# Kernel optimization log

Hardware: AMD Instinct MI355X
Metric: run time of the kernel (lower is better)

The kernel has to match this reference:

```python
import jax, jax.numpy as jnp
import numpy as np

S, B, H, NH = 2048, 1, 2048, 16
HD = H // NH
ROTARY_BASE = 10000.0
MASK_FILL = -10000.0  # gpt2_attention_mask_func fill value


def _rotate_half(x):
    x1, x2 = jnp.split(x, 2, axis=-1)
    return jnp.concatenate((-x2, x1), axis=-1)


def _rotary_cos_sin(seq_len, dim, dtype):
    inv_freq = 1.0 / (ROTARY_BASE ** (jnp.arange(0, dim, 2, dtype=jnp.float32) / dim))
    t = jnp.arange(seq_len, dtype=jnp.float32)
    freqs = t[:, None] * inv_freq[None, :]          # [s, dim/2]
    emb = jnp.concatenate((freqs, freqs), axis=-1)  # [s, dim]
    # shape [s, 1, 1, dim] to broadcast over (batch, heads)
    return jnp.cos(emb)[:, None, None, :].astype(dtype), jnp.sin(emb)[:, None, None, :].astype(dtype)


def setup_inputs() -> dict:
    key = jax.random.key(0)
    k0, k1, k2 = jax.random.split(key, 3)
    hidden_states = jax.random.normal(k0, (S, B, H), dtype=jnp.float32) * 0.02
    # causal mask: True = masked (upper triangle above diagonal)
    attention_mask = jnp.triu(jnp.ones((1, 1, S, S), dtype=bool), k=1)
    w_qkv = jax.random.normal(k1, (3 * H, H), dtype=jnp.float32) * 0.02
    b_qkv = jnp.zeros((3 * H,), dtype=jnp.float32)
    w_dense = jax.random.normal(k2, (H, H), dtype=jnp.float32) * 0.02
    return {"hidden_states": hidden_states, "attention_mask": attention_mask,
            "w_qkv": w_qkv, "b_qkv": b_qkv, "w_dense": w_dense}


def reference(hidden_states, attention_mask, w_qkv, b_qkv, w_dense):
    s, b, h = hidden_states.shape
    # fused QKV projection: [s, b, 3h]
    mixed = jnp.einsum('sbh,oh->sbo', hidden_states, w_qkv) + b_qkv
    mixed = mixed.reshape(s, b, NH, 3 * HD)
    q, k, v = jnp.split(mixed, 3, axis=-1)  # each [s, b, nh, hd]
    # rotary embedding (rotary_pct == 1 -> full head dim)
    cos, sin = _rotary_cos_sin(s, HD, q.dtype)
    q = q * cos + _rotate_half(q) * sin
    k = k * cos + _rotate_half(k) * sin
    # scaled QK^T: [b, nh, sq, sk]
    norm_factor = jnp.asarray(1.0 / np.sqrt(HD), dtype=q.dtype)
    scores = jnp.einsum('sbnd,tbnd->bnst', q, k) * norm_factor
    scores = jnp.where(attention_mask, jnp.asarray(MASK_FILL, scores.dtype), scores)
    probs = jax.nn.softmax(scores.astype(jnp.float32), axis=-1).astype(scores.dtype)
    # PV: [s, b, nh, hd]
    ctx = jnp.einsum('bnst,tbnd->sbnd', probs, v)
    ctx = ctx.reshape(s, b, h)
    # RowParallelLinear with skip_bias_add: bias returned separately (not added)
    out = jnp.einsum('sbh,oh->sbo', ctx, w_dense)
    return out
```

## Files before the change

kernel.cpp:

```cpp
#include <hip/hip_runtime.h>


#define S_LEN 2048
#define NHEAD 16
#define HDIM  128
#define HID   2048
#define H3    6144

typedef short bf16x8 __attribute__((ext_vector_type(8)));
typedef float f32x4  __attribute__((ext_vector_type(4)));

__device__ __forceinline__ float bf2f(ushort u) {
  union { float f; unsigned int i; } v; v.i = ((unsigned int)u) << 16; return v.f;
}
__device__ __forceinline__ ushort f2bf(float f) {
  union { float f; unsigned int i; } v; v.f = f;
  unsigned int r = v.i + 0x7fffu + ((v.i >> 16) & 1u);
  return (ushort)(r >> 16);
}
__device__ __forceinline__ int4 cvt8(const float* p) {
  float4 a = *(const float4*)p, b = *(const float4*)(p + 4);
  union { ushort u[8]; int4 v; } r;
  r.u[0] = f2bf(a.x); r.u[1] = f2bf(a.y); r.u[2] = f2bf(a.z); r.u[3] = f2bf(a.w);
  r.u[4] = f2bf(b.x); r.u[5] = f2bf(b.y); r.u[6] = f2bf(b.z); r.u[7] = f2bf(b.w);
  return r.v;
}

typedef __attribute__((address_space(1))) const unsigned int gu32;
typedef __attribute__((address_space(3))) unsigned int lu32;
__device__ __forceinline__ void async16(const void* g, void* l) {
  __builtin_amdgcn_global_load_lds((gu32*)g, (lu32*)l, 16, 0, 0);
}

__global__ __launch_bounds__(256) void cvt_bf16(const float* __restrict__ src,
                                                ushort* __restrict__ dst, int n8) {
  int i = blockIdx.x * 256 + threadIdx.x;
  if (i < n8) *(int4*)&dst[(size_t)i * 8] = cvt8(&src[(size_t)i * 8]);
}

template<int BM, int BN, bool HAS_BIAS, bool OUT_F32>
__global__ __launch_bounds__(256) void gemm_async(const ushort* __restrict__ A,
                                                  const ushort* __restrict__ W,
                                                  const float* __restrict__ bias,
                                                  void* __restrict__ Cv,
                                                  int N, int K, int AS, int AH) {
  __shared__ __align__(16) ushort As[BM * 32];
  __shared__ __align__(16) ushort Ws[BN * 32];
  const int tid  = threadIdx.x;
  const int lane = tid & 63;
  const int w    = tid >> 6;
  const int wr   = w >> 1, wc = w & 1;
  const int quad = lane >> 4, ln15 = lane & 15;
  const int tm = blockIdx.y * BM, tn = blockIdx.x * BN;
  constexpr int MI = BM / 32, NJ = BN / 32;

  f32x4 acc[MI][NJ];
#pragma unroll
  for (int i = 0; i < MI; ++i)
#pragma unroll
    for (int j = 0; j < NJ; ++j) acc[i][j] = (f32x4){0.f, 0.f, 0.f, 0.f};

  const int lrow = lane >> 2;
  const int lcol = (lane & 3) * 8;

  for (int k0 = 0; k0 < K; k0 += 32) {
    const int aoff = (k0 >> 7) * AH + (k0 & 127) + lcol;
    for (int r = w; r < (BM + BN) / 16; r += 4) {
      if (r < BM / 16) {
        async16(&A[(size_t)(tm + r * 16 + lrow) * AS + aoff], &As[r * 16 * 32]);
      } else {
        const int rb = r - BM / 16;
        async16(&W[(size_t)(tn + rb * 16 + lrow) * K + k0 + lcol], &Ws[rb * 16 * 32]);
      }
    }
    __syncthreads();
    bf16x8 af[MI], bw[NJ];
#pragma unroll
    for (int i = 0; i < MI; ++i)
      af[i] = *(const bf16x8*)&As[((BM / 2) * wr + 16 * i + ln15) * 32 + quad * 8];
#pragma unroll
    for (int j = 0; j < NJ; ++j)
      bw[j] = *(const bf16x8*)&Ws[((BN / 2) * wc + 16 * j + ln15) * 32 + quad * 8];
#pragma unroll
    for (int i = 0; i < MI; ++i)
#pragma unroll
      for (int j = 0; j < NJ; ++j)
        acc[i][j] = __builtin_amdgcn_mfma_f32_16x16x32_bf16(af[i], bw[j], acc[i][j], 0, 0, 0);
    __syncthreads();
  }

#pragma unroll
  for (int i = 0; i < MI; ++i)
#pragma unroll
    for (int j = 0; j < NJ; ++j) {
      int col = tn + (BN / 2) * wc + 16 * j + ln15;
      float badd = HAS_BIAS ? bias[col] : 0.0f;
#pragma unroll
      for (int r = 0; r < 4; ++r) {
        int row = tm + (BM / 2) * wr + 16 * i + 4 * quad + r;
        float val = acc[i][j][r] + badd;
        if (OUT_F32) ((float*)Cv)[(size_t)row * N + col] = val;
        else         ((ushort*)Cv)[(size_t)row * N + col] = f2bf(val);
      }
    }
}

template<bool A_F32, bool HAS_BIAS, bool OUT_F32>
__global__ __launch_bounds__(256) void gemm_bt(const void* __restrict__ Av,
                                               const float* __restrict__ W,
                                               const float* __restrict__ bias,
                                               void* __restrict__ Cv,
                                               int M, int N, int K, int AS, int AH) {
  __shared__ __align__(16) ushort As[128 * 40];
  __shared__ __align__(16) ushort Ws[128 * 40];
  const int tid  = threadIdx.x;
  const int lane = tid & 63;
  const int w    = tid >> 6;
  const int wr   = w >> 1, wc = w & 1;
  const int quad = lane >> 4, ln15 = lane & 15;
  const int tm = blockIdx.y * 128, tn = blockIdx.x * 128;

  f32x4 acc[4][4];
#pragma unroll
  for (int i = 0; i < 4; ++i)
#pragma unroll
    for (int j = 0; j < 4; ++j) acc[i][j] = (f32x4){0.f, 0.f, 0.f, 0.f};

  const int row0 = tid >> 2, row1 = row0 + 64;
  const int kp   = (tid & 3) * 8;

  for (int k0 = 0; k0 < K; k0 += 32) {
    const int ka   = k0 + kp;
    const int aoff = (ka >> 7) * AH + (ka & 127);
    if (A_F32) {
      const float* A = (const float*)Av;
      *(int4*)&As[row0 * 40 + kp] = cvt8(&A[(size_t)(tm + row0) * AS + aoff]);
      *(int4*)&As[row1 * 40 + kp] = cvt8(&A[(size_t)(tm + row1) * AS + aoff]);
    } else {
      const ushort* A = (const ushort*)Av;
      *(int4*)&As[row0 * 40 + kp] = *(const int4*)&A[(size_t)(tm + row0) * AS + aoff];
      *(int4*)&As[row1 * 40 + kp] = *(const int4*)&A[(size_t)(tm + row1) * AS + aoff];
    }
    *(int4*)&Ws[row0 * 40 + kp] = cvt8(&W[(size_t)(tn + row0) * K + ka]);
    *(int4*)&Ws[row1 * 40 + kp] = cvt8(&W[(size_t)(tn + row1) * K + ka]);
    __syncthreads();
    bf16x8 af[4], bw[4];
#pragma unroll
    for (int i = 0; i < 4; ++i)
      af[i] = *(const bf16x8*)&As[(64 * wr + 16 * i + ln15) * 40 + quad * 8];
#pragma unroll
    for (int j = 0; j < 4; ++j)
      bw[j] = *(const bf16x8*)&Ws[(64 * wc + 16 * j + ln15) * 40 + quad * 8];
#pragma unroll
    for (int i = 0; i < 4; ++i)
#pragma unroll
      for (int j = 0; j < 4; ++j)
        acc[i][j] = __builtin_amdgcn_mfma_f32_16x16x32_bf16(af[i], bw[j], acc[i][j], 0, 0, 0);
    __syncthreads();
  }

#pragma unroll
  for (int i = 0; i < 4; ++i)
#pragma unroll
    for (int j = 0; j < 4; ++j) {
      int col = tn + 64 * wc + 16 * j + ln15;
      float badd = HAS_BIAS ? bias[col] : 0.0f;
#pragma unroll
      for (int r = 0; r < 4; ++r) {
        int row = tm + 64 * wr + 16 * i + 4 * quad + r;
        float val = acc[i][j][r] + badd;
        if (OUT_F32) ((float*)Cv)[(size_t)row * N + col] = val;
        else         ((ushort*)Cv)[(size_t)row * N + col] = f2bf(val);
      }
    }
}

__global__ __launch_bounds__(256) void rope_kernel(ushort* __restrict__ mixed) {
  int t = blockIdx.x * 256 + threadIdx.x;
  int d = t & 63;
  int n = (t >> 6) & (NHEAD - 1);
  int s = t >> 10;
  ushort* base = mixed + (size_t)s * H3 + n * 384;
  float invf = exp2f((float)d * (-13.287712379549449f / 64.0f));
  float ang = (float)s * invf;
  float si, c; sincosf(ang, &si, &c);
  float q0 = bf2f(base[d]),       q1 = bf2f(base[64 + d]);
  float k0 = bf2f(base[128 + d]), k1 = bf2f(base[192 + d]);
  base[d]       = f2bf(q0 * c - q1 * si);
  base[64 + d]  = f2bf(q1 * c + q0 * si);
  base[128 + d] = f2bf(k0 * c - k1 * si);
  base[192 + d] = f2bf(k1 * c + k0 * si);
}

__global__ __launch_bounds__(256) void v_transpose(const ushort* __restrict__ mixed,
                                                   ushort* __restrict__ vt) {
  __shared__ __align__(16) ushort Vl[64 * 136];
  const int tid = threadIdx.x;
  const int sb = blockIdx.x;
  const int n  = blockIdx.y;
#pragma unroll
  for (int it = 0; it < 4; ++it) {
    int c = tid + it * 256;
    int row = c >> 4, dp = (c & 15) * 8;
    *(int4*)&Vl[row * 136 + dp] =
        *(const int4*)&mixed[(size_t)(sb * 64 + row) * H3 + n * 384 + 256 + dp];
  }
  __syncthreads();
#pragma unroll
  for (int it = 0; it < 4; ++it) {
    int c = tid + it * 256;
    int d = c >> 3, sp = (c & 7) * 8;
    union { ushort u[8]; int4 v; } pk;
#pragma unroll
    for (int e = 0; e < 8; ++e) pk.u[e] = Vl[(sp + e) * 136 + d];
    *(int4*)&vt[((size_t)(n * 128 + d)) * S_LEN + sb * 64 + sp] = pk.v;
  }
}

__global__ __launch_bounds__(256) void attn_kernel(const ushort* __restrict__ mixed,
                                                   const ushort* __restrict__ vt,
                                                   ushort* __restrict__ ctx,
                                                   int CS, int CH) {
  __shared__ __align__(16) ushort Ks[64 * 136];
  __shared__ __align__(16) ushort Vt[128 * 72];
  __shared__ __align__(16) float  Ss[4 * 16 * 68];

  const int tid  = threadIdx.x;
  const int lane = tid & 63;
  const int w    = tid >> 6;
  const int quad = lane >> 4, ln15 = lane & 15;
  const int qb = blockIdx.x;
  const int n  = blockIdx.y;
  const float scale = 0.08838834764831845f;

  bf16x8 aqr[4];
#pragma unroll
  for (int ks = 0; ks < 4; ++ks)
    aqr[ks] = *(const bf16x8*)&mixed[(size_t)(qb * 64 + 16 * w + ln15) * H3 + n * 384
                                     + ks * 32 + quad * 8];

  f32x4 acc_o[8];
#pragma unroll
  for (int jt = 0; jt < 8; ++jt) acc_o[jt] = (f32x4){0.f, 0.f, 0.f, 0.f};
  float m_run[4], l_run[4];
#pragma unroll
  for (int r = 0; r < 4; ++r) { m_run[r] = -1e30f; l_run[r] = 0.0f; }

  float* Ssw = &Ss[w * 16 * 68];

  for (int kt = 0; kt <= qb; ++kt) {
#pragma unroll
    for (int it = 0; it < 4; ++it) {
      int c = tid + it * 256;
      int row = c >> 4, dp = (c & 15) * 8;
      *(int4*)&Ks[row * 136 + dp] =
          *(const int4*)&mixed[(size_t)(kt * 64 + row) * H3 + n * 384 + 128 + dp];
      int d = c >> 3, sp = (c & 7) * 8;
      *(int4*)&Vt[d * 72 + sp] =
          *(const int4*)&vt[((size_t)(n * 128 + d)) * S_LEN + kt * 64 + sp];
    }
    __syncthreads();

    f32x4 sacc[4];
#pragma unroll
    for (int jt = 0; jt < 4; ++jt) sacc[jt] = (f32x4){0.f, 0.f, 0.f, 0.f};
#pragma unroll
    for (int ks = 0; ks < 4; ++ks) {
#pragma unroll
      for (int jt = 0; jt < 4; ++jt) {
        bf16x8 bk = *(const bf16x8*)&Ks[(16 * jt + ln15) * 136 + ks * 32 + quad * 8];
        sacc[jt] = __builtin_amdgcn_mfma_f32_16x16x32_bf16(aqr[ks], bk, sacc[jt], 0, 0, 0);
      }
    }

    float sv[4][4];
    const int ig = qb * 64 + 16 * w + 4 * quad;
#pragma unroll
    for (int jt = 0; jt < 4; ++jt) {
      int jg = kt * 64 + 16 * jt + ln15;
#pragma unroll
      for (int r = 0; r < 4; ++r) {
        float x = sacc[jt][r] * scale;
        sv[jt][r] = (jg > ig + r) ? -10000.0f : x;
      }
    }

    float tmx[4];
#pragma unroll
    for (int r = 0; r < 4; ++r)
      tmx[r] = fmaxf(fmaxf(sv[0][r], sv[1][r]), fmaxf(sv[2][r], sv[3][r]));
#pragma unroll
    for (int m = 1; m <= 8; m <<= 1)
#pragma unroll
      for (int r = 0; r < 4; ++r) tmx[r] = fmaxf(tmx[r], __shfl_xor(tmx[r], m));

    float alpha[4];
#pragma unroll
    for (int r = 0; r < 4; ++r) {
      float m_new = fmaxf(m_run[r], tmx[r]);
      alpha[r] = __expf(m_run[r] - m_new);
      m_run[r] = m_new;
    }

    float ps[4] = {0.f, 0.f, 0.f, 0.f};
#pragma unroll
    for (int jt = 0; jt < 4; ++jt)
#pragma unroll
      for (int r = 0; r < 4; ++r) {
        float p = __expf(sv[jt][r] - m_run[r]);
        Ssw[(4 * quad + r) * 68 + 16 * jt + ln15] = p;
        ps[r] += p;
      }
#pragma unroll
    for (int m = 1; m <= 8; m <<= 1)
#pragma unroll
      for (int r = 0; r < 4; ++r) ps[r] += __shfl_xor(ps[r], m);
#pragma unroll
    for (int r = 0; r < 4; ++r) l_run[r] = alpha[r] * l_run[r] + ps[r];

#pragma unroll
    for (int jt = 0; jt < 8; ++jt)
#pragma unroll
      for (int r = 0; r < 4; ++r) acc_o[jt][r] *= alpha[r];
#pragma unroll
    for (int ks = 0; ks < 2; ++ks) {
      const float* pp = &Ssw[ln15 * 68 + ks * 32 + quad * 8];
      float4 p0 = *(const float4*)(pp);
      float4 p1 = *(const float4*)(pp + 4);
      bf16x8 ap;
      ap[0] = (short)f2bf(p0.x); ap[1] = (short)f2bf(p0.y);
      ap[2] = (short)f2bf(p0.z); ap[3] = (short)f2bf(p0.w);
      ap[4] = (short)f2bf(p1.x); ap[5] = (short)f2bf(p1.y);
      ap[6] = (short)f2bf(p1.z); ap[7] = (short)f2bf(p1.w);
#pragma unroll
      for (int jt = 0; jt < 8; ++jt) {
        bf16x8 bv = *(const bf16x8*)&Vt[(16 * jt + ln15) * 72 + ks * 32 + quad * 8];
        acc_o[jt] = __builtin_amdgcn_mfma_f32_16x16x32_bf16(ap, bv, acc_o[jt], 0, 0, 0);
      }
    }
    __syncthreads();
  }

  float rinv[4];
#pragma unroll
  for (int r = 0; r < 4; ++r) rinv[r] = 1.0f / l_run[r];
#pragma unroll
  for (int jt = 0; jt < 8; ++jt)
#pragma unroll
    for (int r = 0; r < 4; ++r) {
      int row = qb * 64 + 16 * w + 4 * quad + r;
      int col = 16 * jt + ln15;
      ctx[(size_t)row * CS + n * CH + col] = f2bf(acc_o[jt][r] * rinv[r]);
    }
}

extern "C" void kernel_launch(void* const* d_in, const int* in_sizes, int n_in,
                              void* d_out, int out_size, void* d_ws, size_t ws_size,
                              hipStream_t stream) {
  const float* hidden  = (const float*)d_in[0];
  const float* w_qkv   = (const float*)d_in[2];
  const float* b_qkv   = (const float*)d_in[3];
  const float* w_dense = (const float*)d_in[4];
  float* out = (float*)d_out;

  char* ws = (char*)d_ws;

  const size_t wq_b    = (size_t)H3 * HID * 2;
  const size_t h_b     = (size_t)S_LEN * HID * 2;
  const size_t mixed_b = (size_t)S_LEN * H3 * 2;
  const size_t vt_b    = (size_t)NHEAD * HDIM * S_LEN * 2;
  const size_t fast_need = wq_b + h_b + mixed_b + vt_b;

  if (ws_size >= fast_need) {
    ushort* WQ    = (ushort*)ws;
    ushort* Hbf   = (ushort*)(ws + wq_b);
    ushort* mixed = (ushort*)(ws + wq_b + h_b);
    ushort* vt    = (ushort*)(ws + wq_b + h_b + mixed_b);
    ushort* WD    = WQ;
    ushort* ctx   = mixed;

    cvt_bf16<<<2048, 256, 0, stream>>>(hidden, Hbf, S_LEN * HID / 8);
    cvt_bf16<<<6144, 256, 0, stream>>>(w_qkv, WQ, H3 * HID / 8);
    gemm_async<128, 128, true, false><<<dim3(48, 16), 256, 0, stream>>>(
        Hbf, WQ, b_qkv, mixed, H3, HID, HID, 128);
    rope_kernel<<<8192, 256, 0, stream>>>(mixed);
    v_transpose<<<dim3(32, 16), 256, 0, stream>>>(mixed, vt);
    attn_kernel<<<dim3(32, 16), 256, 0, stream>>>(mixed, vt, ctx, H3, 384);
    cvt_bf16<<<2048, 256, 0, stream>>>(w_dense, WD, HID * HID / 8);
    gemm_async<64, 128, false, true><<<dim3(16, 32), 256, 0, stream>>>(
        ctx, WD, nullptr, out, HID, HID, H3, 384);
  } else {
    ushort* mixed = (ushort*)ws;
    ushort* vt    = (ushort*)(ws + mixed_b);
    const bool big = ws_size >= mixed_b + vt_b + (size_t)S_LEN * HID * 2;
    ushort* ctx = big ? (ushort*)(ws + mixed_b + vt_b) : mixed;
    const int CS = big ? HID  : H3;
    const int CH = big ? HDIM : 384;

    gemm_bt<true, true, false><<<dim3(48, 16), 256, 0, stream>>>(
        hidden, w_qkv, b_qkv, mixed, S_LEN, H3, HID, HID, HDIM);
    rope_kernel<<<8192, 256, 0, stream>>>(mixed);
    v_transpose<<<dim3(32, 16), 256, 0, stream>>>(mixed, vt);
    attn_kernel<<<dim3(32, 16), 256, 0, stream>>>(mixed, vt, ctx, CS, CH);
    gemm_bt<false, false, true><<<dim3(16, 16), 256, 0, stream>>>(
        ctx, w_dense, nullptr, out, S_LEN, HID, HID, CS, CH);
  }
}
```

Before: 354.4 us.

## Prefetch K tiles in registers, read V directly from global, swizzle LDS, skip rescale

The attention loop now prefetches the next K tile into registers while the current tile is computed. Each wave loads its V^T fragments straight from global memory into registers instead of staging them through shared memory. Padded LDS layouts are replaced with XOR-swizzled ones for K and the probability scratch. The online-softmax rescale of the accumulator and running sum is skipped when no row max grows anywhere in the wavefront. These changes cut LDS traffic and footprint and hide global latency, at the cost of more registers (16 bf16x8 V fragments plus the K prefetch) and redundant V global loads across the four waves.

```diff
diff --git a/kernel.cpp b/kernel.cpp
--- a/kernel.cpp
+++ b/kernel.cpp
@@ -221,9 +221,8 @@
                                                    const ushort* __restrict__ vt,
                                                    ushort* __restrict__ ctx,
                                                    int CS, int CH) {
-  __shared__ __align__(16) ushort Ks[64 * 136];
-  __shared__ __align__(16) ushort Vt[128 * 72];
-  __shared__ __align__(16) float  Ss[4 * 16 * 68];
+  __shared__ __align__(16) ushort Ks[64 * 128];
+  __shared__ __align__(16) float  Ss[4 * 16 * 64];
 
   const int tid  = threadIdx.x;
   const int lane = tid & 63;
@@ -246,20 +245,39 @@
 #pragma unroll
   for (int r = 0; r < 4; ++r) { m_run[r] = -1e30f; l_run[r] = 0.0f; }
 
-  float* Ssw = &Ss[w * 16 * 68];
+  float* Ssw = &Ss[w * 16 * 64];
+
+  const int krow = tid >> 4;
+  const int kcol = (tid & 15) * 8;
+  const ushort* Kg = mixed + n * 384 + 128;
+  const ushort* Vg = vt + (size_t)n * 128 * S_LEN;
+
+  int4 kreg[4];
+#pragma unroll
+  for (int it = 0; it < 4; ++it)
+    kreg[it] = *(const int4*)&Kg[(size_t)(krow + 16 * it) * H3 + kcol];
 
   for (int kt = 0; kt <= qb; ++kt) {
+    bf16x8 vreg[16];
+#pragma unroll
+    for (int ks = 0; ks < 2; ++ks)
+#pragma unroll
+      for (int jt = 0; jt < 8; ++jt)
+        vreg[ks * 8 + jt] = *(const bf16x8*)&Vg[(size_t)(16 * jt + ln15) * S_LEN
+                                                + kt * 64 + ks * 32 + quad * 8];
+
 #pragma unroll
     for (int it = 0; it < 4; ++it) {
-      int c = tid + it * 256;
-      int row = c >> 4, dp = (c & 15) * 8;
-      *(int4*)&Ks[row * 136 + dp] =
-          *(const int4*)&mixed[(size_t)(kt * 64 + row) * H3 + n * 384 + 128 + dp];
-      int d = c >> 3, sp = (c & 7) * 8;
-      *(int4*)&Vt[d * 72 + sp] =
-          *(const int4*)&vt[((size_t)(n * 128 + d)) * S_LEN + kt * 64 + sp];
-    }
-    __syncthreads();
+      int row = krow + 16 * it;
+      *(int4*)&Ks[row * 128 + (kcol ^ ((row & 7) << 3))] = kreg[it];
+    }
+    __syncthreads();
+
+    if (kt < qb) {
+#pragma unroll
+      for (int it = 0; it < 4; ++it)
+        kreg[it] = *(const int4*)&Kg[(size_t)((kt + 1) * 64 + krow + 16 * it) * H3 + kcol];
+    }
 
     f32x4 sacc[4];
 #pragma unroll
@@ -268,7 +286,8 @@
     for (int ks = 0; ks < 4; ++ks) {
 #pragma unroll
       for (int jt = 0; jt < 4; ++jt) {
-        bf16x8 bk = *(const bf16x8*)&Ks[(16 * jt + ln15) * 136 + ks * 32 + quad * 8];
+        bf16x8 bk = *(const bf16x8*)&Ks[(16 * jt + ln15) * 128
+                                        + ((ks * 32 + quad * 8) ^ ((ln15 & 7) << 3))];
         sacc[jt] = __builtin_amdgcn_mfma_f32_16x16x32_bf16(aqr[ks], bk, sacc[jt], 0, 0, 0);
       }
     }
@@ -294,12 +313,18 @@
 #pragma unroll
       for (int r = 0; r < 4; ++r) tmx[r] = fmaxf(tmx[r], __shfl_xor(tmx[r], m));
 
-    float alpha[4];
-#pragma unroll
-    for (int r = 0; r < 4; ++r) {
-      float m_new = fmaxf(m_run[r], tmx[r]);
-      alpha[r] = __expf(m_run[r] - m_new);
-      m_run[r] = m_new;
+    bool grow = (tmx[0] > m_run[0]) | (tmx[1] > m_run[1]) |
+                (tmx[2] > m_run[2]) | (tmx[3] > m_run[3]);
+    if (__any(grow)) {
+#pragma unroll
+      for (int r = 0; r < 4; ++r) {
+        float m_new = fmaxf(m_run[r], tmx[r]);
+        float alpha = __expf(m_run[r] - m_new);
+        m_run[r] = m_new;
+        l_run[r] *= alpha;
+#pragma unroll
+        for (int jt = 0; jt < 8; ++jt) acc_o[jt][r] *= alpha;
+      }
     }
 
     float ps[4] = {0.f, 0.f, 0.f, 0.f};
@@ -308,7 +333,8 @@
 #pragma unroll
       for (int r = 0; r < 4; ++r) {
         float p = __expf(sv[jt][r] - m_run[r]);
-        Ssw[(4 * quad + r) * 68 + 16 * jt + ln15] = p;
+        int row = 4 * quad + r;
+        Ssw[row * 64 + ((16 * jt + ln15) ^ ((row & 7) << 2))] = p;
         ps[r] += p;
       }
 #pragma unroll
@@ -316,27 +342,23 @@
 #pragma unroll
       for (int r = 0; r < 4; ++r) ps[r] += __shfl_xor(ps[r], m);
 #pragma unroll
-    for (int r = 0; r < 4; ++r) l_run[r] = alpha[r] * l_run[r] + ps[r];
-
-#pragma unroll
-    for (int jt = 0; jt < 8; ++jt)
-#pragma unroll
-      for (int r = 0; r < 4; ++r) acc_o[jt][r] *= alpha[r];
+    for (int r = 0; r < 4; ++r) l_run[r] += ps[r];
+
 #pragma unroll
     for (int ks = 0; ks < 2; ++ks) {
-      const float* pp = &Ssw[ln15 * 68 + ks * 32 + quad * 8];
-      float4 p0 = *(const float4*)(pp);
-      float4 p1 = *(const float4*)(pp + 4);
+      int base = ks * 32 + quad * 8;
+      int cc = (ln15 & 7) << 2;
+      float4 p0 = *(const float4*)&Ssw[ln15 * 64 + (base ^ cc)];
+      float4 p1 = *(const float4*)&Ssw[ln15 * 64 + ((base + 4) ^ cc)];
       bf16x8 ap;
       ap[0] = (short)f2bf(p0.x); ap[1] = (short)f2bf(p0.y);
       ap[2] = (short)f2bf(p0.z); ap[3] = (short)f2bf(p0.w);
       ap[4] = (short)f2bf(p1.x); ap[5] = (short)f2bf(p1.y);
       ap[6] = (short)f2bf(p1.z); ap[7] = (short)f2bf(p1.w);
 #pragma unroll
-      for (int jt = 0; jt < 8; ++jt) {
-        bf16x8 bv = *(const bf16x8*)&Vt[(16 * jt + ln15) * 72 + ks * 32 + quad * 8];
-        acc_o[jt] = __builtin_amdgcn_mfma_f32_16x16x32_bf16(ap, bv, acc_o[jt], 0, 0, 0);
-      }
+      for (int jt = 0; jt < 8; ++jt)
+        acc_o[jt] = __builtin_amdgcn_mfma_f32_16x16x32_bf16(ap, vreg[ks * 8 + jt],
+                                                            acc_o[jt], 0, 0, 0);
     }
     __syncthreads();
   }
```

After: 457.5 us. 1.29x slower.

## Double-buffer K tiles with async LDS loads, swizzle layout, store P as bf16

Applied to the files above, without the earlier changes.

The attention kernel now stages K and V tiles into LDS through async global-to-LDS copies (async16). K is double-buffered so the next tile's load overlaps the current QK^T compute, and V is issued at the top of each iteration. Both use an XOR swizzle in place of padding to avoid bank conflicts. Probabilities are converted to bf16 once when written to LDS rather than when read, which halves the scratch traffic. Launch bounds now request 2 blocks per CU. The V buffer is single and reused, so correctness depends on the placement of the barriers and on async completion semantics.

```diff
diff --git a/kernel.cpp b/kernel.cpp
--- a/kernel.cpp
+++ b/kernel.cpp
@@ -217,13 +217,13 @@
   }
 }
 
-__global__ __launch_bounds__(256) void attn_kernel(const ushort* __restrict__ mixed,
-                                                   const ushort* __restrict__ vt,
-                                                   ushort* __restrict__ ctx,
-                                                   int CS, int CH) {
-  __shared__ __align__(16) ushort Ks[64 * 136];
-  __shared__ __align__(16) ushort Vt[128 * 72];
-  __shared__ __align__(16) float  Ss[4 * 16 * 68];
+__global__ __launch_bounds__(256, 2) void attn_kernel(const ushort* __restrict__ mixed,
+                                                      const ushort* __restrict__ vt,
+                                                      ushort* __restrict__ ctx,
+                                                      int CS, int CH) {
+  __shared__ __align__(16) ushort Ks[2][64 * 128];
+  __shared__ __align__(16) ushort Vs[128 * 64];
+  __shared__ __align__(16) ushort Ss[4][16 * 72];
 
   const int tid  = threadIdx.x;
   const int lane = tid & 63;
@@ -233,6 +233,9 @@
   const int n  = blockIdx.y;
   const float scale = 0.08838834764831845f;
 
+  const ushort* Kg = mixed + n * 384 + 128;
+  const ushort* Vg = vt + (size_t)n * 128 * S_LEN;
+
   bf16x8 aqr[4];
 #pragma unroll
   for (int ks = 0; ks < 4; ++ks)
@@ -246,20 +249,36 @@
 #pragma unroll
   for (int r = 0; r < 4; ++r) { m_run[r] = -1e30f; l_run[r] = 0.0f; }
 
-  float* Ssw = &Ss[w * 16 * 68];
+  ushort* Ssw = Ss[w];
+
+  const int krow = lane >> 4, kcs = lane & 15;
+  const int vrow = lane >> 3, vcs = lane & 7;
+  const int swz  = ln15 & 7;
+
+#define STAGE_K(KT, BUF)                                                        \
+  { _Pragma("unroll")                                                           \
+    for (int i = 0; i < 4; ++i) {                                               \
+      int kr = w * 16 + i * 4 + krow;                                           \
+      int kcl = kcs ^ (kr & 7);                                                 \
+      async16(&Kg[(size_t)((KT) * 64 + kr) * H3 + kcl * 8],                     \
+              &Ks[BUF][(w * 16 + i * 4) * 128]);                                \
+    } }
+#define STAGE_V(KT)                                                             \
+  { _Pragma("unroll")                                                           \
+    for (int i = 0; i < 4; ++i) {                                               \
+      int vr = w * 32 + i * 8 + vrow;                                           \
+      int vcl = vcs ^ (vr & 7);                                                 \
+      async16(&Vg[(size_t)vr * S_LEN + (KT) * 64 + vcl * 8],                    \
+              &Vs[(w * 32 + i * 8) * 64]);                                      \
+    } }
+
+  int cur = 0;
+  STAGE_K(0, 0);
+  __syncthreads();
 
   for (int kt = 0; kt <= qb; ++kt) {
-#pragma unroll
-    for (int it = 0; it < 4; ++it) {
-      int c = tid + it * 256;
-      int row = c >> 4, dp = (c & 15) * 8;
-      *(int4*)&Ks[row * 136 + dp] =
-          *(const int4*)&mixed[(size_t)(kt * 64 + row) * H3 + n * 384 + 128 + dp];
-      int d = c >> 3, sp = (c & 7) * 8;
-      *(int4*)&Vt[d * 72 + sp] =
-          *(const int4*)&vt[((size_t)(n * 128 + d)) * S_LEN + kt * 64 + sp];
-    }
-    __syncthreads();
+    STAGE_V(kt);
+    if (kt < qb) STAGE_K(kt + 1, cur ^ 1);
 
     f32x4 sacc[4];
 #pragma unroll
@@ -268,7 +287,8 @@
     for (int ks = 0; ks < 4; ++ks) {
 #pragma unroll
       for (int jt = 0; jt < 4; ++jt) {
-        bf16x8 bk = *(const bf16x8*)&Ks[(16 * jt + ln15) * 136 + ks * 32 + quad * 8];
+        bf16x8 bk = *(const bf16x8*)&Ks[cur][(16 * jt + ln15) * 128
+                                            + ((ks * 4 + quad) ^ swz) * 8];
         sacc[jt] = __builtin_amdgcn_mfma_f32_16x16x32_bf16(aqr[ks], bk, sacc[jt], 0, 0, 0);
       }
     }
@@ -308,7 +328,7 @@
 #pragma unroll
       for (int r = 0; r < 4; ++r) {
         float p = __expf(sv[jt][r] - m_run[r]);
-        Ssw[(4 * quad + r) * 68 + 16 * jt + ln15] = p;
+        Ssw[(4 * quad + r) * 72 + 16 * jt + ln15] = f2bf(p);
         ps[r] += p;
       }
 #pragma unroll
@@ -322,24 +342,25 @@
     for (int jt = 0; jt < 8; ++jt)
 #pragma unroll
       for (int r = 0; r < 4; ++r) acc_o[jt][r] *= alpha[r];
+
+    __syncthreads();
+
 #pragma unroll
     for (int ks = 0; ks < 2; ++ks) {
-      const float* pp = &Ssw[ln15 * 68 + ks * 32 + quad * 8];
-      float4 p0 = *(const float4*)(pp);
-      float4 p1 = *(const float4*)(pp + 4);
-      bf16x8 ap;
-      ap[0] = (short)f2bf(p0.x); ap[1] = (short)f2bf(p0.y);
-      ap[2] = (short)f2bf(p0.z); ap[3] = (short)f2bf(p0.w);
-      ap[4] = (short)f2bf(p1.x); ap[5] = (short)f2bf(p1.y);
-      ap[6] = (short)f2bf(p1.z); ap[7] = (short)f2bf(p1.w);
+      bf16x8 ap = *(const bf16x8*)&Ssw[ln15 * 72 + ks * 32 + quad * 8];
 #pragma unroll
       for (int jt = 0; jt < 8; ++jt) {
-        bf16x8 bv = *(const bf16x8*)&Vt[(16 * jt + ln15) * 72 + ks * 32 + quad * 8];
+        bf16x8 bv = *(const bf16x8*)&Vs[(16 * jt + ln15) * 64
+                                        + ((ks * 4 + quad) ^ swz) * 8];
         acc_o[jt] = __builtin_amdgcn_mfma_f32_16x16x32_bf16(ap, bv, acc_o[jt], 0, 0, 0);
       }
     }
-    __syncthreads();
-  }
+
+    __syncthreads();
+    cur ^= 1;
+  }
+#undef STAGE_K
+#undef STAGE_V
 
   float rinv[4];
 #pragma unroll
```

New measurement: 345.1 us. 2.6% less time.
